# Kernel optimization log

Measured on AMD Instinct MI355X. Metric: run time of the kernel, lower is better.

The kernel has to match this reference:

```python
import jax, jax.numpy as jnp
import numpy as np

N = 4096        # n_nodes
IN_DIM = 256    # input_dim
HID = 256       # hidden_dim
OUT_DIM = 128   # output_dim
NUM_HOPS = 3
ALPHA = 0.2     # LeakyReLU slope
EDGE_P = 0.002  # adjacency density (avg degree ~8)


def setup_inputs() -> dict:
    key = jax.random.key(0)
    ks = jax.random.split(key, 7)
    X = jax.random.normal(ks[0], (N, IN_DIM), dtype=jnp.float32)
    # sparse binary adjacency with self-loops (so every softmax row is non-empty)
    A = (jax.random.uniform(ks[1], (N, N)) < EDGE_P).astype(jnp.float32)
    A = A.at[jnp.arange(N), jnp.arange(N)].set(1.0)
    W_s = jax.random.normal(ks[2], (IN_DIM, HID), dtype=jnp.float32) / np.sqrt(IN_DIM)
    r = jax.random.normal(ks[3], (2 * HID, 1), dtype=jnp.float32) / np.sqrt(2 * HID)
    W_l = jax.random.normal(ks[4], (HID, HID), dtype=jnp.float32) / np.sqrt(HID)
    W_out = jax.random.normal(ks[5], (HID, OUT_DIM), dtype=jnp.float32) / np.sqrt(HID)
    b_out = jnp.zeros((OUT_DIM,), dtype=jnp.float32)
    return {"X": X, "A": A, "W_s": W_s, "r": r, "W_l": W_l,
            "W_out": W_out, "b_out": b_out}


def reference(X, A, W_s, r, W_l, W_out, b_out):
    # ---- ShortDistanceAttention (GAT-style, 1-hop) ----
    Wh = X @ W_s                              # [N, HID]
    # cat([Wh_i, Wh_j]) @ r  ==  Wh @ r[:HID] + (Wh @ r[HID:]).T  (no N*N*2H tensor)
    s_i = Wh @ r[:HID]                        # [N, 1]
    s_j = Wh @ r[HID:]                        # [N, 1]
    e = jax.nn.leaky_relu(s_i + s_j.T, ALPHA) # [N, N]
    e = jnp.where(A != 0, e, -jnp.inf)
    attn = jax.nn.softmax(e, axis=1)
    h = jax.nn.gelu(attn @ Wh, approximate=False)   # [N, HID]

    # ---- LongDistanceAttention k-hop loop ----
    Wa = h @ W_l                              # [N, HID]
    scores = h @ Wa.T                         # [N, N] (loop-invariant in original)
    out = h
    Ak = A
    for k in range(NUM_HOPS):
        sk = jnp.where(Ak != 0, scores, -jnp.inf)
        wk = jax.nn.softmax(sk, axis=1)       # rows non-empty: diag(A^k) > 0
        out = out + wk @ h
        if k + 1 < NUM_HOPS:
            Ak = Ak @ A                       # A^(k+1)
    return out @ W_out + b_out                # [N, OUT_DIM]
```

## Files before the change

### kernel.cpp

```cpp
#include <hip/hip_runtime.h>
#include <cstdint>
#include <cstddef>

typedef unsigned long long u64;
typedef unsigned short u16;
typedef unsigned int u32;
typedef __bf16 bf16x8 __attribute__((ext_vector_type(8)));
typedef float f32x4 __attribute__((ext_vector_type(4)));

#define NN 4096
#define HIDD 256

__device__ __forceinline__ u16 f2bf(float f) {
  unsigned int u = __float_as_uint(f);
  u = u + 0x7FFFu + ((u >> 16) & 1u);
  return (u16)(u >> 16);
}
__device__ __forceinline__ float bf2f(u16 h) {
  return __uint_as_float(((unsigned int)h) << 16);
}
__device__ __forceinline__ float gelu_f(float x) {
  return 0.5f * x * (1.0f + erff(x * 0.70710678118654752f));
}
__device__ __forceinline__ void gload_lds16(const u16* g, u16* l) {
  __builtin_amdgcn_global_load_lds((const __attribute__((address_space(1))) void*)g,
                                   (__attribute__((address_space(3))) void*)l, 16, 0, 0);
}

__global__ __launch_bounds__(256) void k_bitset(const float* __restrict__ A, u64* __restrict__ B1) {
  __shared__ unsigned char nib[4][1024];
  int wv = threadIdx.x >> 6, ln = threadIdx.x & 63;
  int row = blockIdx.x * 4 + wv;
  const float4* ar = (const float4*)(A + (size_t)row * NN);
#pragma unroll
  for (int it = 0; it < 16; ++it) {
    float4 v = ar[it * 64 + ln];
    unsigned n = (v.x != 0.f ? 1u : 0u) | (v.y != 0.f ? 2u : 0u) |
                 (v.z != 0.f ? 4u : 0u) | (v.w != 0.f ? 8u : 0u);
    nib[wv][it * 64 + ln] = (unsigned char)n;
  }
  __syncthreads();
  const u32* np4 = (const u32*)&nib[wv][ln * 16];
  u64 word = 0;
#pragma unroll
  for (int q = 0; q < 4; ++q) {
    u32 four = np4[q];
    u64 part = (u64)(four & 0xFu) | ((u64)((four >> 8) & 0xFu) << 4) |
               ((u64)((four >> 16) & 0xFu) << 8) | ((u64)((four >> 24) & 0xFu) << 12);
    word |= part << (16 * q);
  }
  B1[(size_t)row * 64 + ln] = word;
}

#define MAXE 96
__global__ __launch_bounds__(256) void k_expand(const u64* __restrict__ src,
                                                const u64* __restrict__ base,
                                                u64* __restrict__ dst) {
  __shared__ int idxs[4][MAXE];
  __shared__ int cnts[4];
  int wv = threadIdx.x >> 6, ln = threadIdx.x & 63;
  int row = blockIdx.x * 4 + wv;
  if (ln == 0) cnts[wv] = 0;
  __syncthreads();
  u64 w = src[(size_t)row * 64 + ln];
  while (w) {
    int b = __builtin_ctzll(w);
    w &= w - 1;
    int p = atomicAdd(&cnts[wv], 1);
    if (p < MAXE) idxs[wv][p] = ln * 64 + b;
  }
  __syncthreads();
  int cnt = cnts[wv] < MAXE ? cnts[wv] : MAXE;
  u64 acc = 0;
  int i = 0;
  for (; i + 4 <= cnt; i += 4) {
    u64 a0 = base[(size_t)idxs[wv][i] * 64 + ln];
    u64 a1 = base[(size_t)idxs[wv][i + 1] * 64 + ln];
    u64 a2 = base[(size_t)idxs[wv][i + 2] * 64 + ln];
    u64 a3 = base[(size_t)idxs[wv][i + 3] * 64 + ln];
    acc |= a0 | a1 | a2 | a3;
  }
  for (; i < cnt; ++i) acc |= base[(size_t)idxs[wv][i] * 64 + ln];
  dst[(size_t)row * 64 + ln] = acc;
}

__global__ __launch_bounds__(256) void k_split(const float* __restrict__ src,
                                               u16* __restrict__ dst, int pat) {
  int rrow = blockIdx.x, c = threadIdx.x;
  float x = src[(size_t)rrow * 256 + c];
  u16 hi = f2bf(x);
  u16 lo = f2bf(x - bf2f(hi));
  size_t b = (size_t)rrow * 768 + c;
  dst[b] = hi;
  dst[b + 256] = pat ? lo : hi;
  dst[b + 512] = pat ? hi : lo;
}

__global__ __launch_bounds__(256) void k_split_r2(const float* __restrict__ p,
                                                  u16* __restrict__ dst) {
  int rrow = blockIdx.x, c = threadIdx.x;
  size_t idx = (size_t)rrow * 256 + c;
  const size_t P = (size_t)NN * 256;
  float x = p[idx] + p[idx + P];
  u16 hi = f2bf(x);
  u16 lo = f2bf(x - bf2f(hi));
  size_t b = (size_t)rrow * 768 + c;
  dst[b] = hi;
  dst[b + 256] = hi;
  dst[b + 512] = lo;
}

__global__ __launch_bounds__(256) void k_reduce2(const float* __restrict__ p,
                                                 float* __restrict__ dst) {
  const size_t P4 = (size_t)NN * 64;
  size_t i = (size_t)blockIdx.x * 256 + threadIdx.x;
  const f32x4* a = (const f32x4*)p;
  f32x4 v = a[i];
  f32x4 w = a[i + P4];
  v[0] += w[0]; v[1] += w[1]; v[2] += w[2]; v[3] += w[3];
  ((f32x4*)dst)[i] = v;
}

__global__ __launch_bounds__(256) void k_splitT2(const float* __restrict__ W0,
                                                 const float* __restrict__ W1,
                                                 u16* __restrict__ d0,
                                                 u16* __restrict__ d1) {
  int blk = blockIdx.x;
  const float* W = blk < 256 ? W0 : W1;
  u16* dst = blk < 256 ? d0 : d1;
  int n = blk & 255, k = threadIdx.x;
  float x = W[(size_t)k * 256 + n];
  u16 hi = f2bf(x);
  u16 lo = f2bf(x - bf2f(hi));
  size_t b = (size_t)n * 768 + k;
  dst[b] = hi;
  dst[b + 256] = hi;
  dst[b + 512] = lo;
}

__global__ __launch_bounds__(256) void gemm_nt(const u16* __restrict__ A,
                                               const u16* __restrict__ B,
                                               float* __restrict__ C,
                                               int M, int N, int K) {
  __shared__ __align__(16) u16 sA[128 * 32];
  __shared__ __align__(16) u16 sB[128 * 32];
  const int tid = threadIdx.x;
  const int wave = tid >> 6, lane = tid & 63;
  const int wr = wave >> 1, wc = wave & 1;

  int bx = blockIdx.x, by = blockIdx.y;
  {
    int nwg = gridDim.x * gridDim.y;
    if (gridDim.z == 1 && (nwg & 7) == 0) {
      int bid = by * gridDim.x + bx;
      int cpx = nwg >> 3;
      bid = (bid & 7) * cpx + (bid >> 3);
      bx = bid % gridDim.x;
      by = bid / gridDim.x;
    }
  }

  const int rowBase = by * 128;
  const int colBase = bx * 128;
  const int kchunk = K / gridDim.z;
  const int k0 = blockIdx.z * kchunk;
  float* Cp = C + (size_t)blockIdx.z * M * N;

  const int srow = lane >> 2;
  const int skoff = (lane & 3) * 8;
  const int fr = lane & 15;
  const int fk = (lane >> 4) * 8;

  f32x4 acc[4][4] = {};

  for (int kt = k0; kt < k0 + kchunk; kt += 32) {
    for (int c = wave; c < 8; c += 4) {
      const u16* ga = A + (size_t)(rowBase + c * 16 + srow) * K + kt + skoff;
      gload_lds16(ga, &sA[c * 512]);
      const u16* gb = B + (size_t)(colBase + c * 16 + srow) * K + kt + skoff;
      gload_lds16(gb, &sB[c * 512]);
    }
    __syncthreads();
    bf16x8 af[4], bfr[4];
#pragma unroll
    for (int m = 0; m < 4; ++m)
      af[m] = *(const bf16x8*)&sA[(wr * 64 + m * 16 + fr) * 32 + fk];
#pragma unroll
    for (int n = 0; n < 4; ++n)
      bfr[n] = *(const bf16x8*)&sB[(wc * 64 + n * 16 + fr) * 32 + fk];
#pragma unroll
    for (int m = 0; m < 4; ++m)
#pragma unroll
      for (int n = 0; n < 4; ++n)
        acc[m][n] = __builtin_amdgcn_mfma_f32_16x16x32_bf16(af[m], bfr[n], acc[m][n], 0, 0, 0);
    __syncthreads();
  }
#pragma unroll
  for (int m = 0; m < 4; ++m)
#pragma unroll
    for (int n = 0; n < 4; ++n) {
      int r0 = rowBase + wr * 64 + m * 16 + (lane >> 4) * 4;
      int c0 = colBase + wc * 64 + n * 16 + fr;
#pragma unroll
      for (int r = 0; r < 4; ++r)
        Cp[(size_t)(r0 + r) * N + c0] = acc[m][n][r];
    }
}

__global__ __launch_bounds__(256) void gemm64_nt(const u16* __restrict__ A,
                                                 const u16* __restrict__ B,
                                                 float* __restrict__ C,
                                                 int M, int N, int K) {
  __shared__ __align__(16) u16 sA[64 * 32];
  __shared__ __align__(16) u16 sB[64 * 32];
  const int tid = threadIdx.x;
  const int wave = tid >> 6, lane = tid & 63;
  const int wr = wave >> 1, wc = wave & 1;
  const int rowBase = blockIdx.y * 64;
  const int colBase = blockIdx.x * 64;
  const int kchunk = K / gridDim.z;
  const int k0 = blockIdx.z * kchunk;
  float* Cp = C + (size_t)blockIdx.z * M * N;

  const int srow = lane >> 2;
  const int skoff = (lane & 3) * 8;
  const int fr = lane & 15;
  const int fk = (lane >> 4) * 8;

  f32x4 acc[2][2] = {};

  for (int kt = k0; kt < k0 + kchunk; kt += 32) {
    const u16* ga = A + (size_t)(rowBase + wave * 16 + srow) * K + kt + skoff;
    gload_lds16(ga, &sA[wave * 512]);
    const u16* gb = B + (size_t)(colBase + wave * 16 + srow) * K + kt + skoff;
    gload_lds16(gb, &sB[wave * 512]);
    __syncthreads();
    bf16x8 af[2], bfr[2];
#pragma unroll
    for (int m = 0; m < 2; ++m)
      af[m] = *(const bf16x8*)&sA[(wr * 32 + m * 16 + fr) * 32 + fk];
#pragma unroll
    for (int n = 0; n < 2; ++n)
      bfr[n] = *(const bf16x8*)&sB[(wc * 32 + n * 16 + fr) * 32 + fk];
#pragma unroll
    for (int m = 0; m < 2; ++m)
#pragma unroll
      for (int n = 0; n < 2; ++n)
        acc[m][n] = __builtin_amdgcn_mfma_f32_16x16x32_bf16(af[m], bfr[n], acc[m][n], 0, 0, 0);
    __syncthreads();
  }
#pragma unroll
  for (int m = 0; m < 2; ++m)
#pragma unroll
    for (int n = 0; n < 2; ++n) {
      int r0 = rowBase + wr * 32 + m * 16 + (lane >> 4) * 4;
      int c0 = colBase + wc * 32 + n * 16 + fr;
#pragma unroll
      for (int r = 0; r < 4; ++r)
        Cp[(size_t)(r0 + r) * N + c0] = acc[m][n][r];
    }
}

__global__ __launch_bounds__(256) void k_sisj(const float* __restrict__ Wh,
                                              const float* __restrict__ r,
                                              float* __restrict__ s) {
  int wv = threadIdx.x >> 6, ln = threadIdx.x & 63;
  int row = blockIdx.x * 4 + wv;
  const float4 wh = *(const float4*)&Wh[(size_t)row * 256 + ln * 4];
  const float4 ri = *(const float4*)&r[ln * 4];
  const float4 rj = *(const float4*)&r[256 + ln * 4];
  float pi = wh.x * ri.x + wh.y * ri.y + wh.z * ri.z + wh.w * ri.w;
  float pj = wh.x * rj.x + wh.y * rj.y + wh.z * rj.z + wh.w * rj.w;
  for (int o = 32; o; o >>= 1) { pi += __shfl_xor(pi, o); pj += __shfl_xor(pj, o); }
  if (ln == 0) { s[row] = pi; s[NN + row] = pj; }
}

#define MAXD 128
__global__ __launch_bounds__(256) void k_attn1(const u64* __restrict__ B1,
                                               const float* __restrict__ s,
                                               const float* __restrict__ Wh,
                                               float* __restrict__ h) {
  __shared__ int idxs[4][MAXD];
  __shared__ float ww[4][MAXD];
  __shared__ int cnts[4];
  int wv = threadIdx.x >> 6, ln = threadIdx.x & 63;
  int row = blockIdx.x * 4 + wv;
  if (ln == 0) cnts[wv] = 0;
  __syncthreads();
  u64 w = B1[(size_t)row * 64 + ln];
  while (w) {
    int b = __builtin_ctzll(w);
    w &= w - 1;
    int p = atomicAdd(&cnts[wv], 1);
    if (p < MAXD) idxs[wv][p] = ln * 64 + b;
  }
  __syncthreads();
  int cnt = cnts[wv] < MAXD ? cnts[wv] : MAXD;
  float si = s[row];
  for (int i = ln; i < cnt; i += 64) {
    float v = si + s[NN + idxs[wv][i]];
    ww[wv][i] = v > 0.f ? v : 0.2f * v;
  }
  __syncthreads();
  float mx = -1e30f;
  for (int i = ln; i < cnt; i += 64) mx = fmaxf(mx, ww[wv][i]);
  for (int o = 32; o; o >>= 1) mx = fmaxf(mx, __shfl_xor(mx, o));
  float sm = 0.f;
  for (int i = ln; i < cnt; i += 64) sm += __expf(ww[wv][i] - mx);
  for (int o = 32; o; o >>= 1) sm += __shfl_xor(sm, o);
  float inv = 1.0f / sm;
  for (int i = ln; i < cnt; i += 64) ww[wv][i] = __expf(ww[wv][i] - mx) * inv;
  __syncthreads();
  float a0 = 0, a1 = 0, a2 = 0, a3 = 0;
  for (int t = 0; t < cnt; ++t) {
    float wgt = ww[wv][t];
    const float4 v = *(const float4*)&Wh[(size_t)idxs[wv][t] * 256 + ln * 4];
    a0 = fmaf(wgt, v.x, a0); a1 = fmaf(wgt, v.y, a1);
    a2 = fmaf(wgt, v.z, a2); a3 = fmaf(wgt, v.w, a3);
  }
  float4 o4;
  o4.x = gelu_f(a0); o4.y = gelu_f(a1); o4.z = gelu_f(a2); o4.w = gelu_f(a3);
  *(float4*)&h[(size_t)row * 256 + ln * 4] = o4;
}

__global__ __launch_bounds__(256) void k_transpose(const float* __restrict__ h,
                                                   u16* __restrict__ hT) {
  __shared__ u16 tile[64][65];
  int t = threadIdx.x;
  int bx = blockIdx.x & 3;
  int by = blockIdx.x >> 2;
  for (int rr = (t >> 6); rr < 64; rr += 4)
    tile[rr][t & 63] = f2bf(h[(size_t)(by * 64 + rr) * 256 + bx * 64 + (t & 63)]);
  __syncthreads();
  for (int jj = (t >> 6); jj < 64; jj += 4)
    hT[(size_t)(bx * 64 + jj) * NN + by * 64 + (t & 63)] = tile[t & 63][jj];
}

__global__ __launch_bounds__(256) void k_wc(const float* __restrict__ scores,
                                            const u64* __restrict__ B1,
                                            const u64* __restrict__ B2,
                                            const u64* __restrict__ B3,
                                            u16* __restrict__ Wc) {
  __shared__ u64 sm3[64];
  __shared__ float rmax[4], rsum[4];
  const int t = threadIdx.x;
  const int wv = t >> 6, ln = t & 63;
  const int row = blockIdx.x;
  const size_t rbase = (size_t)row * NN;

  if (t < 64) sm3[t] = B3[(size_t)row * 64 + t];
  f32x4 v[4];
  const f32x4* sp = (const f32x4*)(scores + rbase);
#pragma unroll
  for (int g = 0; g < 4; ++g) v[g] = sp[g * 256 + t];
  u64 w2 = 0, w1 = 0;
  if (wv == 0) {
    w2 = B2[(size_t)row * 64 + ln];
    w1 = B1[(size_t)row * 64 + ln];
  }
  __syncthreads();

  const int wi = t >> 4;
  const int sb = (t & 15) * 4;
  u32 nib[4];
  float mx3 = -3e38f;
#pragma unroll
  for (int g = 0; g < 4; ++g) {
    u64 wrd = sm3[g * 16 + wi];
    u32 half = (sb < 32) ? (u32)wrd : (u32)(wrd >> 32);
    nib[g] = (half >> (sb & 31)) & 0xFu;
#pragma unroll
    for (int j = 0; j < 4; ++j)
      if (nib[g] & (1u << j)) mx3 = fmaxf(mx3, v[g][j]);
  }
  for (int o = 32; o; o >>= 1) mx3 = fmaxf(mx3, __shfl_xor(mx3, o));
  if (ln == 0) rmax[wv] = mx3;

  float mx2 = -3e38f, mx1 = -3e38f;
  if (wv == 0) {
    u64 w = w2;
    while (w) {
      int b = __builtin_ctzll(w); w &= w - 1;
      float sc = scores[rbase + ln * 64 + b];
      mx2 = fmaxf(mx2, sc);
      if (w1 & (1ull << b)) mx1 = fmaxf(mx1, sc);
    }
    for (int o = 32; o; o >>= 1) {
      mx2 = fmaxf(mx2, __shfl_xor(mx2, o));
      mx1 = fmaxf(mx1, __shfl_xor(mx1, o));
    }
  }
  __syncthreads();
  mx3 = fmaxf(fmaxf(rmax[0], rmax[1]), fmaxf(rmax[2], rmax[3]));

  float s3 = 0.f;
#pragma unroll
  for (int g = 0; g < 4; ++g)
#pragma unroll
    for (int j = 0; j < 4; ++j) {
      float e = __expf(v[g][j] - mx3);
      e = (nib[g] & (1u << j)) ? e : 0.f;
      v[g][j] = e;
      s3 += e;
    }
  for (int o = 32; o; o >>= 1) s3 += __shfl_xor(s3, o);
  if (ln == 0) rsum[wv] = s3;

  float s2 = 1.f, s1 = 1.f;
  if (wv == 0) {
    float s2p = 0.f, s1p = 0.f;
    u64 w = w2;
    while (w) {
      int b = __builtin_ctzll(w); w &= w - 1;
      float sc = scores[rbase + ln * 64 + b];
      s2p += __expf(sc - mx2);
      if (w1 & (1ull << b)) s1p += __expf(sc - mx1);
    }
    for (int o = 32; o; o >>= 1) {
      s2p += __shfl_xor(s2p, o);
      s1p += __shfl_xor(s1p, o);
    }
    s2 = s2p; s1 = s1p;
  }
  __syncthreads();
  s3 = rsum[0] + rsum[1] + rsum[2] + rsum[3];
  float inv3 = 1.0f / s3;

#pragma unroll
  for (int g = 0; g < 4; ++g) {
    u16 o0 = f2bf(v[g][0] * inv3), o1 = f2bf(v[g][1] * inv3);
    u16 o2 = f2bf(v[g][2] * inv3), o3 = f2bf(v[g][3] * inv3);
    uint2 pk;
    pk.x = (u32)o0 | ((u32)o1 << 16);
    pk.y = (u32)o2 | ((u32)o3 << 16);
    *(uint2*)&Wc[rbase + (size_t)g * 1024 + t * 4] = pk;
  }
  __syncthreads();

  if (wv == 0) {
    float inv2 = 1.0f / s2, inv1 = 1.0f / s1;
    u64 w = w2;
    while (w) {
      int b = __builtin_ctzll(w); w &= w - 1;
      int c = ln * 64 + b;
      float sc = scores[rbase + c];
      float wgt = __expf(sc - mx3) * inv3 + __expf(sc - mx2) * inv2;
      if (w1 & (1ull << b)) wgt += __expf(sc - mx1) * inv1;
      Wc[rbase + c] = f2bf(wgt);
    }
  }
}

__global__ __launch_bounds__(128) void k_final(const float* __restrict__ h,
                                               const float* __restrict__ tmp,
                                               const float* __restrict__ Wout,
                                               const float* __restrict__ bout,
                                               float* __restrict__ out) {
  __shared__ float rrow[8][256];
  int t = threadIdx.x;
  int row0 = blockIdx.x * 8;
  const size_t P = (size_t)NN * 256;
  for (int i = t; i < 8 * 256; i += 128) {
    int rr = i >> 8, k = i & 255;
    size_t idx = (size_t)(row0 + rr) * 256 + k;
    rrow[rr][k] = h[idx] + tmp[idx] + tmp[idx + P] + tmp[idx + 2 * P] + tmp[idx + 3 * P];
  }
  __syncthreads();
  float b = bout[t];
  float acc[8];
#pragma unroll
  for (int i = 0; i < 8; ++i) acc[i] = b;
  for (int k = 0; k < 256; ++k) {
    float w = Wout[k * 128 + t];
#pragma unroll
    for (int i = 0; i < 8; ++i) acc[i] = fmaf(rrow[i][k], w, acc[i]);
  }
#pragma unroll
  for (int i = 0; i < 8; ++i) out[(size_t)(row0 + i) * 128 + t] = acc[i];
}

extern "C" void kernel_launch(void* const* d_in, const int* in_sizes, int n_in,
                              void* d_out, int out_size, void* d_ws, size_t ws_size,
                              hipStream_t stream) {
  const float* X    = (const float*)d_in[0];
  const float* A    = (const float*)d_in[1];
  const float* W_s  = (const float*)d_in[2];
  const float* r    = (const float*)d_in[3];
  const float* W_l  = (const float*)d_in[4];
  const float* Wout = (const float*)d_in[5];
  const float* bout = (const float*)d_in[6];
  float* out = (float*)d_out;

  char* wp = (char*)d_ws;
  auto take = [&](size_t n) { char* p = wp; wp += (n + 255) & ~(size_t)255; return p; };
  u64* B1     = (u64*)take((size_t)NN * 64 * 8);
  u64* B2     = (u64*)take((size_t)NN * 64 * 8);
  u64* B3     = (u64*)take((size_t)NN * 64 * 8);
  float* Wh   = (float*)take((size_t)NN * 256 * 4);
  float* sv   = (float*)take((size_t)2 * NN * 4);
  float* h    = (float*)take((size_t)NN * 256 * 4);
  u16* hT     = (u16*)take((size_t)256 * NN * 2);
  u16* hsp    = (u16*)take((size_t)NN * 768 * 2);
  u16* Wasp   = (u16*)take((size_t)NN * 768 * 2);
  u16* Xsp    = (u16*)take((size_t)NN * 768 * 2);
  u16* WsT    = (u16*)take((size_t)256 * 768 * 2);
  u16* WlT    = (u16*)take((size_t)256 * 768 * 2);
  float* scores = (float*)take((size_t)NN * NN * 4);
  float* Whp  = scores;
  float* Wap  = scores + (size_t)2 * NN * 256;
  float* tmp  = scores;
  u16* Wc     = (u16*)take((size_t)NN * NN * 2);
  (void)n_in; (void)in_sizes; (void)out_size; (void)ws_size;

  k_bitset<<<NN / 4, 256, 0, stream>>>(A, B1);
  k_expand<<<NN / 4, 256, 0, stream>>>(B1, B1, B2);
  k_expand<<<NN / 4, 256, 0, stream>>>(B1, B2, B3);
  k_splitT2<<<512, 256, 0, stream>>>(W_s, W_l, WsT, WlT);
  k_split<<<NN, 256, 0, stream>>>(X, Xsp, 1);
  gemm64_nt<<<dim3(4, 64, 2), 256, 0, stream>>>(Xsp, WsT, Whp, NN, 256, 768);
  k_reduce2<<<1024, 256, 0, stream>>>(Whp, Wh);
  k_sisj<<<NN / 4, 256, 0, stream>>>(Wh, r, sv);
  k_attn1<<<NN / 4, 256, 0, stream>>>(B1, sv, Wh, h);
  k_split<<<NN, 256, 0, stream>>>(h, hsp, 1);
  k_transpose<<<256, 256, 0, stream>>>(h, hT);
  gemm64_nt<<<dim3(4, 64, 2), 256, 0, stream>>>(hsp, WlT, Wap, NN, 256, 768);
  k_split_r2<<<NN, 256, 0, stream>>>(Wap, Wasp);
  gemm_nt<<<dim3(32, 32, 1), 256, 0, stream>>>(hsp, Wasp, scores, NN, NN, 768);
  k_wc<<<NN, 256, 0, stream>>>(scores, B1, B2, B3, Wc);
  gemm64_nt<<<dim3(4, 64, 4), 256, 0, stream>>>(Wc, hT, tmp, NN, 256, NN);
  k_final<<<NN / 8, 128, 0, stream>>>(h, tmp, Wout, bout, out);
}
```

Before: 289.5 us.

## Fuse prep, reduce+sisj, split+transpose kernels and swizzle GEMM LDS layout

Merges the weight-transpose split and X split into one launch, fuses the split-K reduction with the s_i/s_j dot products, and combines the h hi/lo split with the bf16 transpose into one kernel. This removes several launches and an extra read of Wh and h. It also XOR-swizzles the LDS k-offset in both GEMMs to cut bank conflicts. The new split+transpose runs only 64 blocks, which may underuse the GPU, and the swizzle must stay consistent between the async global-to-LDS store and the fragment reads.

```diff
diff --git a/kernel.cpp b/kernel.cpp
--- a/kernel.cpp
+++ b/kernel.cpp
@@ -84,16 +84,28 @@
   dst[(size_t)row * 64 + ln] = acc;
 }
 
-__global__ __launch_bounds__(256) void k_split(const float* __restrict__ src,
-                                               u16* __restrict__ dst, int pat) {
-  int rrow = blockIdx.x, c = threadIdx.x;
-  float x = src[(size_t)rrow * 256 + c];
-  u16 hi = f2bf(x);
-  u16 lo = f2bf(x - bf2f(hi));
-  size_t b = (size_t)rrow * 768 + c;
-  dst[b] = hi;
-  dst[b + 256] = pat ? lo : hi;
-  dst[b + 512] = pat ? hi : lo;
+__global__ __launch_bounds__(256) void k_prep(const float* __restrict__ W0,
+                                              const float* __restrict__ W1,
+                                              const float* __restrict__ X,
+                                              u16* __restrict__ d0,
+                                              u16* __restrict__ d1,
+                                              u16* __restrict__ dx) {
+  int blk = blockIdx.x, t = threadIdx.x;
+  if (blk < 512) {
+    const float* W = blk < 256 ? W0 : W1;
+    u16* dst = blk < 256 ? d0 : d1;
+    int n = blk & 255;
+    float x = W[(size_t)t * 256 + n];
+    u16 hi = f2bf(x), lo = f2bf(x - bf2f(hi));
+    size_t b = (size_t)n * 768 + t;
+    dst[b] = hi; dst[b + 256] = hi; dst[b + 512] = lo;
+  } else {
+    int rrow = blk - 512;
+    float x = X[(size_t)rrow * 256 + t];
+    u16 hi = f2bf(x), lo = f2bf(x - bf2f(hi));
+    size_t b = (size_t)rrow * 768 + t;
+    dx[b] = hi; dx[b + 256] = lo; dx[b + 512] = hi;
+  }
 }
 
 __global__ __launch_bounds__(256) void k_split_r2(const float* __restrict__ p,
@@ -110,32 +122,25 @@
   dst[b + 512] = lo;
 }
 
-__global__ __launch_bounds__(256) void k_reduce2(const float* __restrict__ p,
-                                                 float* __restrict__ dst) {
-  const size_t P4 = (size_t)NN * 64;
-  size_t i = (size_t)blockIdx.x * 256 + threadIdx.x;
-  const f32x4* a = (const f32x4*)p;
-  f32x4 v = a[i];
-  f32x4 w = a[i + P4];
-  v[0] += w[0]; v[1] += w[1]; v[2] += w[2]; v[3] += w[3];
-  ((f32x4*)dst)[i] = v;
-}
-
-__global__ __launch_bounds__(256) void k_splitT2(const float* __restrict__ W0,
-                                                 const float* __restrict__ W1,
-                                                 u16* __restrict__ d0,
-                                                 u16* __restrict__ d1) {
-  int blk = blockIdx.x;
-  const float* W = blk < 256 ? W0 : W1;
-  u16* dst = blk < 256 ? d0 : d1;
-  int n = blk & 255, k = threadIdx.x;
-  float x = W[(size_t)k * 256 + n];
-  u16 hi = f2bf(x);
-  u16 lo = f2bf(x - bf2f(hi));
-  size_t b = (size_t)n * 768 + k;
-  dst[b] = hi;
-  dst[b + 256] = hi;
-  dst[b + 512] = lo;
+__global__ __launch_bounds__(256) void k_reduce2_sisj(const float* __restrict__ p,
+                                                      const float* __restrict__ r,
+                                                      float* __restrict__ Wh,
+                                                      float* __restrict__ s) {
+  int wv = threadIdx.x >> 6, ln = threadIdx.x & 63;
+  int row = blockIdx.x * 4 + wv;
+  const size_t P = (size_t)NN * 256;
+  size_t idx = (size_t)row * 256 + ln * 4;
+  float4 a = *(const float4*)&p[idx];
+  float4 b = *(const float4*)&p[idx + P];
+  float4 wh;
+  wh.x = a.x + b.x; wh.y = a.y + b.y; wh.z = a.z + b.z; wh.w = a.w + b.w;
+  *(float4*)&Wh[idx] = wh;
+  const float4 ri = *(const float4*)&r[ln * 4];
+  const float4 rj = *(const float4*)&r[256 + ln * 4];
+  float pi = wh.x * ri.x + wh.y * ri.y + wh.z * ri.z + wh.w * ri.w;
+  float pj = wh.x * rj.x + wh.y * rj.y + wh.z * rj.z + wh.w * rj.w;
+  for (int o = 32; o; o >>= 1) { pi += __shfl_xor(pi, o); pj += __shfl_xor(pj, o); }
+  if (ln == 0) { s[row] = pi; s[NN + row] = pj; }
 }
 
 __global__ __launch_bounds__(256) void gemm_nt(const u16* __restrict__ A,
@@ -167,9 +172,9 @@
   float* Cp = C + (size_t)blockIdx.z * M * N;
 
   const int srow = lane >> 2;
-  const int skoff = (lane & 3) * 8;
+  const int skoff = ((lane & 3) ^ (srow & 3)) * 8;
   const int fr = lane & 15;
-  const int fk = (lane >> 4) * 8;
+  const int fk = ((lane >> 4) * 8) ^ ((fr & 3) << 3);
 
   f32x4 acc[4][4] = {};
 
@@ -223,9 +228,9 @@
   float* Cp = C + (size_t)blockIdx.z * M * N;
 
   const int srow = lane >> 2;
-  const int skoff = (lane & 3) * 8;
+  const int skoff = ((lane & 3) ^ (srow & 3)) * 8;
   const int fr = lane & 15;
-  const int fk = (lane >> 4) * 8;
+  const int fk = ((lane >> 4) * 8) ^ ((fr & 3) << 3);
 
   f32x4 acc[2][2] = {};
 
@@ -259,20 +264,6 @@
       for (int r = 0; r < 4; ++r)
         Cp[(size_t)(r0 + r) * N + c0] = acc[m][n][r];
     }
-}
-
-__global__ __launch_bounds__(256) void k_sisj(const float* __restrict__ Wh,
-                                              const float* __restrict__ r,
-                                              float* __restrict__ s) {
-  int wv = threadIdx.x >> 6, ln = threadIdx.x & 63;
-  int row = blockIdx.x * 4 + wv;
-  const float4 wh = *(const float4*)&Wh[(size_t)row * 256 + ln * 4];
-  const float4 ri = *(const float4*)&r[ln * 4];
-  const float4 rj = *(const float4*)&r[256 + ln * 4];
-  float pi = wh.x * ri.x + wh.y * ri.y + wh.z * ri.z + wh.w * ri.w;
-  float pj = wh.x * rj.x + wh.y * rj.y + wh.z * rj.z + wh.w * rj.w;
-  for (int o = 32; o; o >>= 1) { pi += __shfl_xor(pi, o); pj += __shfl_xor(pj, o); }
-  if (ln == 0) { s[row] = pi; s[NN + row] = pj; }
 }
 
 #define MAXD 128
@@ -323,17 +314,34 @@
   *(float4*)&h[(size_t)row * 256 + ln * 4] = o4;
 }
 
-__global__ __launch_bounds__(256) void k_transpose(const float* __restrict__ h,
-                                                   u16* __restrict__ hT) {
-  __shared__ u16 tile[64][65];
+__global__ __launch_bounds__(256) void k_splitH_T(const float* __restrict__ h,
+                                                  u16* __restrict__ hsp,
+                                                  u16* __restrict__ hT) {
+  __shared__ u16 tile[64][260];
   int t = threadIdx.x;
-  int bx = blockIdx.x & 3;
-  int by = blockIdx.x >> 2;
-  for (int rr = (t >> 6); rr < 64; rr += 4)
-    tile[rr][t & 63] = f2bf(h[(size_t)(by * 64 + rr) * 256 + bx * 64 + (t & 63)]);
-  __syncthreads();
-  for (int jj = (t >> 6); jj < 64; jj += 4)
-    hT[(size_t)(bx * 64 + jj) * NN + by * 64 + (t & 63)] = tile[t & 63][jj];
+  int row0 = blockIdx.x * 64;
+#pragma unroll
+  for (int it = 0; it < 16; ++it) {
+    int idx = it * 256 + t;
+    int rr = idx >> 6;
+    int c4 = (idx & 63) * 4;
+    float4 v = *(const float4*)&h[(size_t)(row0 + rr) * 256 + c4];
+    u16 h0 = f2bf(v.x), h1 = f2bf(v.y), h2 = f2bf(v.z), h3 = f2bf(v.w);
+    u16 l0 = f2bf(v.x - bf2f(h0)), l1 = f2bf(v.y - bf2f(h1));
+    u16 l2 = f2bf(v.z - bf2f(h2)), l3 = f2bf(v.w - bf2f(h3));
+    ushort4 hv = {h0, h1, h2, h3}, lv = {l0, l1, l2, l3};
+    size_t b = (size_t)(row0 + rr) * 768 + c4;
+    *(ushort4*)&hsp[b] = hv;
+    *(ushort4*)&hsp[b + 256] = lv;
+    *(ushort4*)&hsp[b + 512] = hv;
+    *(ushort4*)&tile[rr][c4] = hv;
+  }
+  __syncthreads();
+#pragma unroll
+  for (int it = 0; it < 64; ++it) {
+    int col = it * 4 + (t >> 6);
+    hT[(size_t)col * NN + row0 + (t & 63)] = tile[t & 63][col];
+  }
 }
 
 __global__ __launch_bounds__(256) void k_wc(const float* __restrict__ scores,
@@ -515,14 +523,11 @@
   k_bitset<<<NN / 4, 256, 0, stream>>>(A, B1);
   k_expand<<<NN / 4, 256, 0, stream>>>(B1, B1, B2);
   k_expand<<<NN / 4, 256, 0, stream>>>(B1, B2, B3);
-  k_splitT2<<<512, 256, 0, stream>>>(W_s, W_l, WsT, WlT);
-  k_split<<<NN, 256, 0, stream>>>(X, Xsp, 1);
+  k_prep<<<512 + NN, 256, 0, stream>>>(W_s, W_l, X, WsT, WlT, Xsp);
   gemm64_nt<<<dim3(4, 64, 2), 256, 0, stream>>>(Xsp, WsT, Whp, NN, 256, 768);
-  k_reduce2<<<1024, 256, 0, stream>>>(Whp, Wh);
-  k_sisj<<<NN / 4, 256, 0, stream>>>(Wh, r, sv);
+  k_reduce2_sisj<<<NN / 4, 256, 0, stream>>>(Whp, r, Wh, sv);
   k_attn1<<<NN / 4, 256, 0, stream>>>(B1, sv, Wh, h);
-  k_split<<<NN, 256, 0, stream>>>(h, hsp, 1);
-  k_transpose<<<256, 256, 0, stream>>>(h, hT);
+  k_splitH_T<<<64, 256, 0, stream>>>(h, hsp, hT);
   gemm64_nt<<<dim3(4, 64, 2), 256, 0, stream>>>(hsp, WlT, Wap, NN, 256, 768);
   k_split_r2<<<NN, 256, 0, stream>>>(Wap, Wasp);
   gemm_nt<<<dim3(32, 32, 1), 256, 0, stream>>>(hsp, Wasp, scores, NN, NN, 768);
```

Measured after the change: 285.2 us. About the same (-1.5%).
